# Optimization experiments

Hardware: AMD Instinct MI355X
Metric: run time of the kernel (lower is better)

## Reference

```python
import math
import jax, jax.numpy as jnp
import numpy as np

B, T, D_MODEL, H, D = 2, 1024, 1024, 16, 64
NUM_LEVELS = int(math.ceil(math.log2(T + 1))) + 1  # 12 for max_seq_len=1024


def _fenwick_level(idx):
    return (idx & -idx).bit_length() - 1


def build_fenwick_masks(T, num_levels):
    """NumPy replica of the torch build_fenwick_masks; returns [L, T, T] float32."""
    j_to_nodes = {}
    for j in range(1, T + 1):
        nodes = []
        idx = j
        while idx <= T:
            nodes.append((idx, _fenwick_level(idx)))
            idx += idx & -idx
        j_to_nodes[j] = nodes
    t_to_query_nodes = {}
    for t in range(1, T + 1):
        s = set()
        idx = t
        while idx > 0:
            s.add(idx)
            idx -= idx & -idx
        t_to_query_nodes[t] = s
    masks = np.zeros((num_levels, T, T), dtype=np.float32)
    for t in range(1, T + 1):
        qn = t_to_query_nodes[t]
        for j in range(1, t + 1):
            for node_idx, node_level in j_to_nodes[j]:
                if node_idx in qn:
                    masks[min(node_level, num_levels - 1), t - 1, j - 1] = 1.0
                    break
    return masks


def setup_inputs() -> dict:
    key = jax.random.key(0)
    ks = jax.random.split(key, 8)
    s = 0.02
    return {
        "x": jax.random.normal(ks[0], (B, T, D_MODEL), jnp.float32),
        "qw": jax.random.normal(ks[1], (D_MODEL, H * D), jnp.float32) * s,
        "qb": jnp.zeros((H * D,), jnp.float32),
        "kw": jax.random.normal(ks[2], (D_MODEL, H * D), jnp.float32) * s,
        "kb": jnp.zeros((H * D,), jnp.float32),
        "vw": jax.random.normal(ks[3], (D_MODEL, H * D), jnp.float32) * s,
        "vb": jnp.zeros((H * D,), jnp.float32),
        "lw": jax.random.normal(ks[4], (D_MODEL, H * NUM_LEVELS), jnp.float32) * s,
        "lb": jnp.zeros((H * NUM_LEVELS,), jnp.float32),
        "ow": jax.random.normal(ks[5], (H * D, D_MODEL), jnp.float32) * s,
        "ob": jnp.zeros((D_MODEL,), jnp.float32),
        "level_masks": jnp.asarray(build_fenwick_masks(T, NUM_LEVELS)),
    }


def reference(x, qw, qb, kw, kb, vw, vb, lw, lb, ow, ob, level_masks):
    b, t, _ = x.shape
    phi = lambda a: jax.nn.elu(a) + 1.0  # ELU+1 feature map
    # projections -> [B, H, T, D]
    Q = (x @ qw + qb).reshape(b, t, H, D).transpose(0, 2, 1, 3)
    K = (x @ kw + kb).reshape(b, t, H, D).transpose(0, 2, 1, 3)
    V = (x @ vw + vb).reshape(b, t, H, D).transpose(0, 2, 1, 3)
    Qp, Kp = phi(Q), phi(K)
    # per-level mixing weights: [B, H, T, L]
    logits = (x @ lw + lb).reshape(b, t, H, NUM_LEVELS).transpose(0, 2, 1, 3)
    w = jax.nn.softmax(logits, axis=-1)
    # scores are level-independent in the original; compute once
    S = jnp.einsum('bhid,bhjd->bhij', Qp, Kp)
    # sum_l w_l * mask_l folded into one weighted mask: [B, H, T, T]
    Mw = jnp.einsum('bhil,lij->bhij', w, level_masks)
    Sm = S * Mw
    num = jnp.einsum('bhij,bhjd->bhid', Sm, V)
    den = jnp.maximum(jnp.sum(Sm, axis=-1, keepdims=True), 1e-6)
    out = (num / den).transpose(0, 2, 1, 3).reshape(b, t, H * D)
    return out @ ow + ob
```

## Files before the change

### kernel.cpp

```cpp
#include <hip/hip_runtime.h>
#include <math.h>

typedef __bf16 bf16;
typedef __attribute__((ext_vector_type(4))) __bf16 bf16x4;
typedef __attribute__((ext_vector_type(8))) __bf16 bf16x8;
typedef __attribute__((ext_vector_type(4))) float f32x4;

#define B_SZ 2
#define T_SZ 1024
#define DM_SZ 1024
#define H_SZ 16
#define D_SZ 64
#define L_SZ 12
#define M_ROWS 2048
#define N_PAD 3328

__device__ __forceinline__ f32x4 mfma_16x16x32(bf16x8 a, bf16x8 b, f32x4 c) {
  return __builtin_amdgcn_mfma_f32_16x16x32_bf16(a, b, c, 0, 0, 0);
}

__device__ __forceinline__ void gload_lds16(const bf16* g, bf16* l) {
  __builtin_amdgcn_global_load_lds((const __attribute__((address_space(1))) void*)g,
                                   (__attribute__((address_space(3))) void*)l,
                                   16, 0, 0);
}

__global__ __launch_bounds__(256) void k_prep(
    const float* __restrict__ x, bf16* __restrict__ xb,
    const float* __restrict__ qw, const float* __restrict__ kw,
    const float* __restrict__ vw, const float* __restrict__ ow,
    const float* __restrict__ lw,
    bf16* __restrict__ wqkvT, bf16* __restrict__ owT) {
  const int u = blockIdx.x;
  const int t = threadIdx.x;
  if (u >= 1072) {
    const size_t base = (size_t)(u - 1072) * 8192 + t * 32;
#pragma unroll
    for (int c = 0; c < 4; ++c) {
      const float* p = x + base + c * 8;
      f32x4 a = *(const f32x4*)p;
      f32x4 b = *(const f32x4*)(p + 4);
      bf16x8 o;
#pragma unroll
      for (int e = 0; e < 4; ++e) { o[e] = (bf16)a[e]; o[e + 4] = (bf16)b[e]; }
      *(bf16x8*)(xb + base + c * 8) = o;
    }
    return;
  }
  __shared__ __align__(16) bf16 tile[64][66];
  const float* in; bf16* out; int C = 1024, tx, ty;
  if (u < 1024) {
    const int z = u >> 8, id = u & 255;
    tx = id & 15; ty = id >> 4;
    if (z == 0)      { in = qw; out = wqkvT; }
    else if (z == 1) { in = kw; out = wqkvT + (size_t)1024 * DM_SZ; }
    else if (z == 2) { in = vw; out = wqkvT + (size_t)2048 * DM_SZ; }
    else             { in = ow; out = owT; }
  } else {
    const int id = u - 1024;
    tx = id % 3; ty = id / 3;
    in = lw; out = wqkvT + (size_t)3072 * DM_SZ; C = 192;
  }
  const int tc = tx * 64, tr = ty * 64;
  const int r = t >> 2;
  const int c4 = (t & 3) << 4;
  const float* src = in + (size_t)(tr + r) * C + tc + c4;
  f32x4 f0 = *(const f32x4*)(src);
  f32x4 f1 = *(const f32x4*)(src + 4);
  f32x4 f2 = *(const f32x4*)(src + 8);
  f32x4 f3 = *(const f32x4*)(src + 12);
#pragma unroll
  for (int e = 0; e < 4; ++e) {
    tile[r][c4 + e]      = (bf16)f0[e];
    tile[r][c4 + 4 + e]  = (bf16)f1[e];
    tile[r][c4 + 8 + e]  = (bf16)f2[e];
    tile[r][c4 + 12 + e] = (bf16)f3[e];
  }
  __syncthreads();
  bf16x8 w0, w1;
#pragma unroll
  for (int e = 0; e < 8; ++e) { w0[e] = tile[c4 + e][r]; w1[e] = tile[c4 + 8 + e][r]; }
  bf16* dst = out + (size_t)(tc + r) * DM_SZ + tr + c4;
  *(bf16x8*)(dst) = w0;
  *(bf16x8*)(dst + 8) = w1;
}

__global__ __launch_bounds__(256) void k_gemm_qkvl(
    const bf16* __restrict__ A, const bf16* __restrict__ Wt,
    const float* __restrict__ qb, const float* __restrict__ kb,
    const float* __restrict__ vb, const float* __restrict__ lb,
    bf16* __restrict__ Qp, bf16* __restrict__ Kp,
    bf16* __restrict__ VTg, float* __restrict__ logit) {
  __shared__ __align__(16) char smem[24576];
  bf16* As = (bf16*)smem;
  bf16* Bs = As + 8192;
  const int nb = blockIdx.x * 64;
  const int mb = blockIdx.y * 128;
  const int t = threadIdx.x;
  const int wv = t >> 6;
  const int lane = t & 63;
  const int l16 = lane & 15;
  const int quad = lane >> 4;
  const int wm = wv * 32;
  const int trow = t >> 3;
  const int tcol = (t & 7) * 8;

  const f32x4 zero4 = {0.f, 0.f, 0.f, 0.f};
  f32x4 acc[2][4];
#pragma unroll
  for (int i = 0; i < 2; ++i)
#pragma unroll
    for (int j = 0; j < 4; ++j) acc[i][j] = zero4;

  const bf16* ag = A + (size_t)(mb + trow) * DM_SZ + tcol;
  const bf16* bg = Wt + (size_t)(nb + trow) * DM_SZ + tcol;

  for (int k0 = 0; k0 < DM_SZ; k0 += 64) {
    __syncthreads();
#pragma unroll
    for (int i = 0; i < 4; ++i)
      gload_lds16(ag + (size_t)i * 32 * DM_SZ + k0, As + i * 2048 + t * 8);
#pragma unroll
    for (int i = 0; i < 2; ++i)
      gload_lds16(bg + (size_t)i * 32 * DM_SZ + k0, Bs + i * 2048 + t * 8);
    __syncthreads();
#pragma unroll
    for (int ks = 0; ks < 2; ++ks) {
      bf16x8 af0 = *(const bf16x8*)(As + (wm + l16) * 64 + ks * 32 + quad * 8);
      bf16x8 af1 = *(const bf16x8*)(As + (wm + 16 + l16) * 64 + ks * 32 + quad * 8);
#pragma unroll
      for (int ni = 0; ni < 4; ++ni) {
        bf16x8 bfr = *(const bf16x8*)(Bs + (ni * 16 + l16) * 64 + ks * 32 + quad * 8);
        acc[0][ni] = mfma_16x16x32(af0, bfr, acc[0][ni]);
        acc[1][ni] = mfma_16x16x32(af1, bfr, acc[1][ni]);
      }
    }
  }

  const int seg = nb >> 10;
  if (seg < 2) {
    const float* bias = seg == 0 ? qb : kb;
    bf16* outp = seg == 0 ? Qp : Kp;
    const int c0 = nb & 1023;
#pragma unroll
    for (int ni = 0; ni < 4; ++ni) {
      const int col = c0 + ni * 16 + l16;
      const float bv = bias[col];
#pragma unroll
      for (int mi = 0; mi < 2; ++mi) {
#pragma unroll
        for (int r = 0; r < 4; ++r) {
          const int row = mb + wm + mi * 16 + quad * 4 + r;
          float v = acc[mi][ni][r] + bv;
          v = (v > 0.f) ? (v + 1.f) : __expf(v);
          outp[(size_t)row * DM_SZ + col] = (bf16)v;
        }
      }
    }
  } else if (seg == 2) {
    bf16* Trt = (bf16*)smem;
    const int cb = nb - 2048;
    __syncthreads();
#pragma unroll
    for (int ni = 0; ni < 4; ++ni) {
      const int nloc = ni * 16 + l16;
      const float bv = vb[cb + nloc];
#pragma unroll
      for (int mi = 0; mi < 2; ++mi) {
        const int mloc = wm + mi * 16 + quad * 4;
        bf16x4 pk;
#pragma unroll
        for (int r = 0; r < 4; ++r) pk[r] = (bf16)(acc[mi][ni][r] + bv);
        *(bf16x4*)&Trt[nloc * 136 + mloc] = pk;
      }
    }
    __syncthreads();
    const int dn = t >> 2, ch = t & 3;
    const int bq = mb >> 10;
    const int m0g = mb & 1023;
    bf16* dst = VTg + ((size_t)(bq * 1024 + cb + dn)) * T_SZ + m0g + ch * 32;
    const bf16* srcl = Trt + dn * 136 + ch * 32;
    *(bf16x8*)(dst) = *(const bf16x8*)(srcl);
    *(bf16x8*)(dst + 8) = *(const bf16x8*)(srcl + 8);
    *(bf16x8*)(dst + 16) = *(const bf16x8*)(srcl + 16);
    *(bf16x8*)(dst + 24) = *(const bf16x8*)(srcl + 24);
  } else {
    const int lc0 = nb - 3072;
#pragma unroll
    for (int ni = 0; ni < 4; ++ni) {
      const int lcol = lc0 + ni * 16 + l16;
      if (lcol < H_SZ * L_SZ) {
        const float bv = lb[lcol];
#pragma unroll
        for (int mi = 0; mi < 2; ++mi) {
#pragma unroll
          for (int r = 0; r < 4; ++r) {
            const int row = mb + wm + mi * 16 + quad * 4 + r;
            logit[(size_t)row * (H_SZ * L_SZ) + lcol] = acc[mi][ni][r] + bv;
          }
        }
      }
    }
  }
}

__global__ __launch_bounds__(256) void k_attn(const bf16* __restrict__ Qp,
                                              const bf16* __restrict__ Kp,
                                              const bf16* __restrict__ VTg,
                                              const float* __restrict__ Lg,
                                              bf16* __restrict__ O) {
  __shared__ __align__(16) bf16 Ks[64][80];
  __shared__ __align__(16) bf16 VTs[64][80];
  __shared__ __align__(16) bf16 Pl[4][16][80];
  __shared__ float Ws[64 * L_SZ];

  const int idx = blockIdx.x;
  const int s = idx >> 5;
  const int bh = idx & 31;
  const int it = (s < 8) ? (15 - s) : (s - 8);
  const int b = bh >> 4;
  const int h = bh & 15;
  const int i0 = it * 64;
  const int t = threadIdx.x;
  const int wv = t >> 6;
  const int lane = t & 63;
  const int l16 = lane & 15;
  const int quad = lane >> 4;
  const int m0 = wv * 16;

  const size_t base_bt = (size_t)b * T_SZ;

  const bf16* qptr = Qp + (base_bt + i0 + m0 + l16) * DM_SZ + h * 64 + quad * 8;
  const bf16x8 aq0 = *(const bf16x8*)(qptr);
  const bf16x8 aq1 = *(const bf16x8*)(qptr + 32);

  if (t < 64) {
    const float* lp = Lg + (base_bt + i0 + t) * (H_SZ * L_SZ) + h * L_SZ;
    float v[L_SZ];
    float m = -1e30f;
#pragma unroll
    for (int l = 0; l < L_SZ; ++l) { v[l] = lp[l]; m = fmaxf(m, v[l]); }
    float sum = 0.f;
#pragma unroll
    for (int l = 0; l < L_SZ; ++l) { v[l] = __expf(v[l] - m); sum += v[l]; }
    const float inv = 1.f / sum;
#pragma unroll
    for (int l = 0; l < L_SZ; ++l) Ws[t * L_SZ + l] = v[l] * inv;
  }

  const f32x4 zero4 = {0.f, 0.f, 0.f, 0.f};
  f32x4 accn[4];
#pragma unroll
  for (int tn = 0; tn < 4; ++tn) accn[tn] = zero4;
  float den[4] = {0.f, 0.f, 0.f, 0.f};

  const int sr = t >> 2;
  const int sc = (t & 3) << 4;
  const int il_base = m0 + quad * 4;

  const bf16* vtrow = VTg + ((size_t)bh * 64 + sr) * T_SZ;

  for (int jt = 0; jt <= it; ++jt) {
    const int j0 = jt * 64;
    const bf16* kpg = Kp + (base_bt + j0 + sr) * DM_SZ + h * 64 + sc;
    bf16x8 k0v = *(const bf16x8*)(kpg);
    bf16x8 k1v = *(const bf16x8*)(kpg + 8);
    const bf16* vpg = vtrow + j0 + sc;
    bf16x8 v0v = *(const bf16x8*)(vpg);
    bf16x8 v1v = *(const bf16x8*)(vpg + 8);
    __syncthreads();
    *(bf16x8*)&Ks[sr][sc] = k0v;
    *(bf16x8*)&Ks[sr][sc + 8] = k1v;
    *(bf16x8*)&VTs[sr][sc] = v0v;
    *(bf16x8*)&VTs[sr][sc + 8] = v1v;
    __syncthreads();

    f32x4 sacc[4];
#pragma unroll
    for (int tn = 0; tn < 4; ++tn) {
      sacc[tn] = zero4;
      bf16x8 bk0 = *(const bf16x8*)&Ks[tn * 16 + l16][quad * 8];
      bf16x8 bk1 = *(const bf16x8*)&Ks[tn * 16 + l16][32 + quad * 8];
      sacc[tn] = mfma_16x16x32(aq0, bk0, sacc[tn]);
      sacc[tn] = mfma_16x16x32(aq1, bk1, sacc[tn]);
    }

    if (jt < it) {
      const int lvlA = 6 + (31 - __clz((unsigned)(it ^ jt)));
      const int lvlB = 6 + (31 - __clz((unsigned)((it + 1) ^ jt)));
      float wrow[4];
#pragma unroll
      for (int r = 0; r < 4; ++r) {
        const int il = il_base + r;
        wrow[r] = Ws[il * L_SZ + ((il == 63) ? lvlB : lvlA)];
      }
#pragma unroll
      for (int tn = 0; tn < 4; ++tn) {
#pragma unroll
        for (int r = 0; r < 4; ++r) {
          const float p = sacc[tn][r] * wrow[r];
          den[r] += p;
          Pl[wv][quad * 4 + r][(tn * 16 + l16) ^ (quad << 4)] = (bf16)p;
        }
      }
    } else {
#pragma unroll
      for (int tn = 0; tn < 4; ++tn) {
#pragma unroll
        for (int r = 0; r < 4; ++r) {
          const int il = il_base + r;
          const int ig = i0 + il;
          const int jg = j0 + tn * 16 + l16;
          float p = 0.f;
          if (jg <= ig) {
            const int lvl = 31 - __clz((unsigned)((ig + 1) ^ jg));
            p = sacc[tn][r] * Ws[il * L_SZ + lvl];
          }
          den[r] += p;
          Pl[wv][quad * 4 + r][(tn * 16 + l16) ^ (quad << 4)] = (bf16)p;
        }
      }
    }

#pragma unroll
    for (int ks = 0; ks < 2; ++ks) {
      bf16x8 apf = *(const bf16x8*)&Pl[wv][l16][(ks * 32 + quad * 8) ^ ((l16 >> 2) << 4)];
#pragma unroll
      for (int tn = 0; tn < 4; ++tn) {
        bf16x8 bvf = *(const bf16x8*)&VTs[tn * 16 + l16][ks * 32 + quad * 8];
        accn[tn] = mfma_16x16x32(apf, bvf, accn[tn]);
      }
    }
  }

#pragma unroll
  for (int r = 0; r < 4; ++r) {
    float d = den[r];
    d += __shfl_xor(d, 1, 64);
    d += __shfl_xor(d, 2, 64);
    d += __shfl_xor(d, 4, 64);
    d += __shfl_xor(d, 8, 64);
    den[r] = fmaxf(d, 1e-6f);
  }

#pragma unroll
  for (int tn = 0; tn < 4; ++tn) {
#pragma unroll
    for (int r = 0; r < 4; ++r) {
      const int il = il_base + r;
      O[(base_bt + i0 + il) * DM_SZ + h * 64 + tn * 16 + l16] =
          (bf16)(accn[tn][r] / den[r]);
    }
  }
}

__global__ __launch_bounds__(256) void k_gemm_out(const bf16* __restrict__ A,
                                                  const bf16* __restrict__ Wt,
                                                  const float* __restrict__ ob,
                                                  float* __restrict__ out) {
  __shared__ __align__(16) bf16 As[64 * 64];
  __shared__ __align__(16) bf16 Bs[64 * 64];
  const int nb = (blockIdx.x & 15) * 64;
  const int mb = (blockIdx.x >> 4) * 64;
  const int t = threadIdx.x;
  const int wv = t >> 6;
  const int lane = t & 63;
  const int l16 = lane & 15;
  const int quad = lane >> 4;
  const int wm = wv * 16;
  const int trow = t >> 3;
  const int tcol = (t & 7) * 8;

  const f32x4 zero4 = {0.f, 0.f, 0.f, 0.f};
  f32x4 acc[4];
#pragma unroll
  for (int j = 0; j < 4; ++j) acc[j] = zero4;

  const bf16* ag = A + (size_t)(mb + trow) * DM_SZ + tcol;
  const bf16* bg = Wt + (size_t)(nb + trow) * DM_SZ + tcol;

  for (int k0 = 0; k0 < DM_SZ; k0 += 64) {
    __syncthreads();
    gload_lds16(ag + k0, As + t * 8);
    gload_lds16(ag + (size_t)32 * DM_SZ + k0, As + 2048 + t * 8);
    gload_lds16(bg + k0, Bs + t * 8);
    gload_lds16(bg + (size_t)32 * DM_SZ + k0, Bs + 2048 + t * 8);
    __syncthreads();
#pragma unroll
    for (int ks = 0; ks < 2; ++ks) {
      bf16x8 af = *(const bf16x8*)(As + (wm + l16) * 64 + ks * 32 + quad * 8);
#pragma unroll
      for (int ni = 0; ni < 4; ++ni) {
        bf16x8 bfr = *(const bf16x8*)(Bs + (ni * 16 + l16) * 64 + ks * 32 + quad * 8);
        acc[ni] = mfma_16x16x32(af, bfr, acc[ni]);
      }
    }
  }
#pragma unroll
  for (int ni = 0; ni < 4; ++ni) {
    const int col = nb + ni * 16 + l16;
    const float bv = ob[col];
#pragma unroll
    for (int r = 0; r < 4; ++r) {
      const int row = mb + wm + quad * 4 + r;
      out[(size_t)row * DM_SZ + col] = acc[ni][r] + bv;
    }
  }
}

extern "C" void kernel_launch(void* const* d_in, const int* in_sizes, int n_in,
                              void* d_out, int out_size, void* d_ws, size_t ws_size,
                              hipStream_t stream) {
  (void)in_sizes; (void)n_in; (void)out_size; (void)ws_size;
  const float* x  = (const float*)d_in[0];
  const float* qw = (const float*)d_in[1];
  const float* qb = (const float*)d_in[2];
  const float* kw = (const float*)d_in[3];
  const float* kb = (const float*)d_in[4];
  const float* vw = (const float*)d_in[5];
  const float* vb = (const float*)d_in[6];
  const float* lw = (const float*)d_in[7];
  const float* lb = (const float*)d_in[8];
  const float* ow = (const float*)d_in[9];
  const float* ob = (const float*)d_in[10];

  char* ws = (char*)d_ws;
  size_t off = 0;
  auto alloc = [&](size_t bytes) -> char* {
    char* p = ws + off;
    off += (bytes + 255) & ~(size_t)255;
    return p;
  };
  bf16* xb     = (bf16*)alloc((size_t)M_ROWS * DM_SZ * 2);
  bf16* wqkvT  = (bf16*)alloc((size_t)N_PAD * DM_SZ * 2);
  bf16* owT    = (bf16*)alloc((size_t)DM_SZ * DM_SZ * 2);
  bf16* Qp     = (bf16*)alloc((size_t)M_ROWS * DM_SZ * 2);
  bf16* Kpb    = (bf16*)alloc((size_t)M_ROWS * DM_SZ * 2);
  bf16* VTg    = (bf16*)alloc((size_t)M_ROWS * DM_SZ * 2);
  bf16* attn   = (bf16*)alloc((size_t)M_ROWS * DM_SZ * 2);
  float* logit = (float*)alloc((size_t)M_ROWS * H_SZ * L_SZ * 4);

  const dim3 blk(256);
  k_prep<<<dim3(1328), blk, 0, stream>>>(x, xb, qw, kw, vw, ow, lw, wqkvT, owT);
  k_gemm_qkvl<<<dim3(N_PAD / 64, M_ROWS / 128), blk, 0, stream>>>(
      xb, wqkvT, qb, kb, vb, lb, Qp, Kpb, VTg, logit);
  k_attn<<<dim3((T_SZ / 64) * B_SZ * H_SZ), blk, 0, stream>>>(Qp, Kpb, VTg, logit, attn);
  k_gemm_out<<<dim3(512), blk, 0, stream>>>(attn, owT, ob, (float*)d_out);
}
```

Measured before the change: 184.1 us.

## Replace off-diagonal attention tiles with Fenwick-block linear-attention state matmuls

Uses the fact that off-diagonal tiles share one weight per row within each Fenwick block. For those blocks the kernel now forms a per-block K^T V state (64x64) and a K column sum, then applies Q·state, instead of computing scores tile by tile. The QKV GEMM also writes a transposed K and per-64-row K sums to support this. The state is rebuilt per block of tiles rather than cached, and it is rounded to bf16 before the Q multiply, which may change accuracy.

After: 191.4 us. 1.04x slower.

```diff
diff --git a/kernel.cpp b/kernel.cpp
--- a/kernel.cpp
+++ b/kernel.cpp
@@ -89,8 +89,8 @@
     const bf16* __restrict__ A, const bf16* __restrict__ Wt,
     const float* __restrict__ qb, const float* __restrict__ kb,
     const float* __restrict__ vb, const float* __restrict__ lb,
-    bf16* __restrict__ Qp, bf16* __restrict__ Kp,
-    bf16* __restrict__ VTg, float* __restrict__ logit) {
+    bf16* __restrict__ Qp, bf16* __restrict__ Kp, bf16* __restrict__ KTg,
+    bf16* __restrict__ VTg, float* __restrict__ K1g, float* __restrict__ logit) {
   __shared__ __align__(16) char smem[24576];
   bf16* As = (bf16*)smem;
   bf16* Bs = As + 8192;
@@ -138,14 +138,12 @@
   }
 
   const int seg = nb >> 10;
-  if (seg < 2) {
-    const float* bias = seg == 0 ? qb : kb;
-    bf16* outp = seg == 0 ? Qp : Kp;
+  if (seg == 0) {
     const int c0 = nb & 1023;
 #pragma unroll
     for (int ni = 0; ni < 4; ++ni) {
       const int col = c0 + ni * 16 + l16;
-      const float bv = bias[col];
+      const float bv = qb[col];
 #pragma unroll
       for (int mi = 0; mi < 2; ++mi) {
 #pragma unroll
@@ -153,9 +151,53 @@
           const int row = mb + wm + mi * 16 + quad * 4 + r;
           float v = acc[mi][ni][r] + bv;
           v = (v > 0.f) ? (v + 1.f) : __expf(v);
-          outp[(size_t)row * DM_SZ + col] = (bf16)v;
+          Qp[(size_t)row * DM_SZ + col] = (bf16)v;
         }
       }
+    }
+  } else if (seg == 1) {
+    bf16* Trt = (bf16*)smem;
+    const int c0 = nb - 1024;
+    const int h = c0 >> 6;
+    const int bq = mb >> 10;
+    const int m0g = mb & 1023;
+    const int bh = bq * 16 + h;
+    __syncthreads();
+#pragma unroll
+    for (int ni = 0; ni < 4; ++ni) {
+      const int nloc = ni * 16 + l16;
+      const float bv = kb[c0 + nloc];
+#pragma unroll
+      for (int mi = 0; mi < 2; ++mi) {
+        const int mloc = wm + mi * 16 + quad * 4;
+        bf16x4 pk;
+#pragma unroll
+        for (int r = 0; r < 4; ++r) {
+          float v = acc[mi][ni][r] + bv;
+          v = (v > 0.f) ? (v + 1.f) : __expf(v);
+          pk[r] = (bf16)v;
+          Kp[(size_t)(mb + mloc + r) * DM_SZ + c0 + nloc] = (bf16)v;
+        }
+        *(bf16x4*)&Trt[nloc * 136 + mloc] = pk;
+      }
+    }
+    __syncthreads();
+    {
+      const int dn = t >> 2, ch = t & 3;
+      bf16* dst = KTg + ((size_t)(bh * 64 + dn)) * T_SZ + m0g + ch * 32;
+      const bf16* srcl = Trt + dn * 136 + ch * 32;
+      *(bf16x8*)(dst) = *(const bf16x8*)(srcl);
+      *(bf16x8*)(dst + 8) = *(const bf16x8*)(srcl + 8);
+      *(bf16x8*)(dst + 16) = *(const bf16x8*)(srcl + 16);
+      *(bf16x8*)(dst + 24) = *(const bf16x8*)(srcl + 24);
+    }
+    if (t < 128) {
+      const int d = t >> 1, half = t & 1;
+      const bf16* rowp = Trt + d * 136 + half * 64;
+      float s = 0.f;
+#pragma unroll
+      for (int e = 0; e < 64; ++e) s += (float)rowp[e];
+      K1g[((size_t)bh * 16 + (m0g >> 6) + half) * 64 + d] = s;
     }
   } else if (seg == 2) {
     bf16* Trt = (bf16*)smem;
@@ -206,19 +248,21 @@
 
 __global__ __launch_bounds__(256) void k_attn(const bf16* __restrict__ Qp,
                                               const bf16* __restrict__ Kp,
+                                              const bf16* __restrict__ KTg,
                                               const bf16* __restrict__ VTg,
+                                              const float* __restrict__ K1g,
                                               const float* __restrict__ Lg,
                                               bf16* __restrict__ O) {
-  __shared__ __align__(16) bf16 Ks[64][80];
-  __shared__ __align__(16) bf16 VTs[64][80];
+  __shared__ float Ws[64 * L_SZ];
+  __shared__ __align__(16) bf16 Mlds[64 * 72];
+  __shared__ float K1Lds[64];
   __shared__ __align__(16) bf16 Pl[4][16][80];
-  __shared__ float Ws[64 * L_SZ];
 
   const int idx = blockIdx.x;
   const int s = idx >> 5;
   const int bh = idx & 31;
   const int it = (s < 8) ? (15 - s) : (s - 8);
-  const int b = bh >> 4;
+  const int b_ = bh >> 4;
   const int h = bh & 15;
   const int i0 = it * 64;
   const int t = threadIdx.x;
@@ -228,7 +272,7 @@
   const int quad = lane >> 4;
   const int m0 = wv * 16;
 
-  const size_t base_bt = (size_t)b * T_SZ;
+  const size_t base_bt = (size_t)b_ * T_SZ;
 
   const bf16* qptr = Qp + (base_bt + i0 + m0 + l16) * DM_SZ + h * 64 + quad * 8;
   const bf16x8 aq0 = *(const bf16x8*)(qptr);
@@ -247,87 +291,130 @@
 #pragma unroll
     for (int l = 0; l < L_SZ; ++l) Ws[t * L_SZ + l] = v[l] * inv;
   }
+  __syncthreads();
 
   const f32x4 zero4 = {0.f, 0.f, 0.f, 0.f};
   f32x4 accn[4];
 #pragma unroll
   for (int tn = 0; tn < 4; ++tn) accn[tn] = zero4;
-  float den[4] = {0.f, 0.f, 0.f, 0.f};
-
-  const int sr = t >> 2;
-  const int sc = (t & 3) << 4;
+  float den_a = 0.f;
+  float dden[4] = {0.f, 0.f, 0.f, 0.f};
+
   const int il_base = m0 + quad * 4;
-
-  const bf16* vtrow = VTg + ((size_t)bh * 64 + sr) * T_SZ;
-
-  for (int jt = 0; jt <= it; ++jt) {
-    const int j0 = jt * 64;
-    const bf16* kpg = Kp + (base_bt + j0 + sr) * DM_SZ + h * 64 + sc;
-    bf16x8 k0v = *(const bf16x8*)(kpg);
-    bf16x8 k1v = *(const bf16x8*)(kpg + 8);
-    const bf16* vpg = vtrow + j0 + sc;
-    bf16x8 v0v = *(const bf16x8*)(vpg);
-    bf16x8 v1v = *(const bf16x8*)(vpg + 8);
-    __syncthreads();
-    *(bf16x8*)&Ks[sr][sc] = k0v;
-    *(bf16x8*)&Ks[sr][sc + 8] = k1v;
-    *(bf16x8*)&VTs[sr][sc] = v0v;
-    *(bf16x8*)&VTs[sr][sc + 8] = v1v;
-    __syncthreads();
-
+  const bf16* c1a = VTg + ((size_t)(bh * 64 + m0 + l16)) * T_SZ;
+  const bf16* c1b = KTg + ((size_t)(bh * 64)) * T_SZ;
+
+#pragma unroll
+  for (int b = 3; b >= 0; --b) {
+    if (!(it & (1 << b))) continue;
+    const int pfx = (it >> (b + 1)) << (b + 1);
+    const int hi = pfx + (1 << b);
+    f32x4 macc[4];
+#pragma unroll
+    for (int ni = 0; ni < 4; ++ni) macc[ni] = zero4;
+    for (int kt = pfx; kt < hi; ++kt) {
+      const int k0 = kt * 64;
+      bf16x8 a0 = *(const bf16x8*)(c1a + k0 + quad * 8);
+      bf16x8 a1 = *(const bf16x8*)(c1a + k0 + 32 + quad * 8);
+#pragma unroll
+      for (int ni = 0; ni < 4; ++ni) {
+        const bf16* brow = c1b + (size_t)(ni * 16 + l16) * T_SZ + k0;
+        bf16x8 b0 = *(const bf16x8*)(brow + quad * 8);
+        bf16x8 b1 = *(const bf16x8*)(brow + 32 + quad * 8);
+        macc[ni] = mfma_16x16x32(a0, b0, macc[ni]);
+        macc[ni] = mfma_16x16x32(a1, b1, macc[ni]);
+      }
+    }
+    __syncthreads();
+#pragma unroll
+    for (int ni = 0; ni < 4; ++ni) {
+#pragma unroll
+      for (int r = 0; r < 4; ++r)
+        Mlds[(m0 + quad * 4 + r) * 72 + ni * 16 + l16] = (bf16)macc[ni][r];
+    }
+    if (t < 64) {
+      float ssum = 0.f;
+      for (int kt = pfx; kt < hi; ++kt)
+        ssum += K1g[((size_t)bh * 16 + kt) * 64 + t];
+      K1Lds[t] = ssum;
+    }
+    __syncthreads();
+    f32x4 tmp[4];
+#pragma unroll
+    for (int ni = 0; ni < 4; ++ni) tmp[ni] = zero4;
+#pragma unroll
+    for (int ks = 0; ks < 2; ++ks) {
+      const bf16x8 aqk = ks ? aq1 : aq0;
+#pragma unroll
+      for (int ni = 0; ni < 4; ++ni) {
+        bf16x8 bm = *(const bf16x8*)(Mlds + (ni * 16 + l16) * 72 + ks * 32 + quad * 8);
+        tmp[ni] = mfma_16x16x32(aqk, bm, tmp[ni]);
+      }
+    }
+    const int lvlA = 6 + b;
+    const int lvlB = 6 + (31 - __clz((unsigned)((it + 1) ^ pfx)));
+    float wrow[4];
+#pragma unroll
+    for (int r = 0; r < 4; ++r) {
+      const int il = il_base + r;
+      wrow[r] = Ws[il * L_SZ + ((il == 63) ? lvlB : lvlA)];
+    }
+#pragma unroll
+    for (int ni = 0; ni < 4; ++ni)
+#pragma unroll
+      for (int r = 0; r < 4; ++r) accn[ni][r] += wrow[r] * tmp[ni][r];
+    {
+      const int ilA = m0 + l16;
+      const float wA = Ws[ilA * L_SZ + ((ilA == 63) ? lvlB : lvlA)];
+      float dot = 0.f;
+#pragma unroll
+      for (int e = 0; e < 8; ++e)
+        dot += (float)aq0[e] * K1Lds[quad * 8 + e] +
+               (float)aq1[e] * K1Lds[32 + quad * 8 + e];
+      dot += __shfl_xor(dot, 16, 64);
+      dot += __shfl_xor(dot, 32, 64);
+      den_a += wA * dot;
+    }
+  }
+
+  {
+    const int j0 = i0;
     f32x4 sacc[4];
 #pragma unroll
+    for (int tn = 0; tn < 4; ++tn) sacc[tn] = zero4;
+#pragma unroll
+    for (int ks = 0; ks < 2; ++ks) {
+      const bf16x8 aqk = ks ? aq1 : aq0;
+#pragma unroll
+      for (int tn = 0; tn < 4; ++tn) {
+        bf16x8 bk = *(const bf16x8*)(Kp + (base_bt + j0 + tn * 16 + l16) * DM_SZ +
+                                     h * 64 + ks * 32 + quad * 8);
+        sacc[tn] = mfma_16x16x32(aqk, bk, sacc[tn]);
+      }
+    }
+#pragma unroll
     for (int tn = 0; tn < 4; ++tn) {
-      sacc[tn] = zero4;
-      bf16x8 bk0 = *(const bf16x8*)&Ks[tn * 16 + l16][quad * 8];
-      bf16x8 bk1 = *(const bf16x8*)&Ks[tn * 16 + l16][32 + quad * 8];
-      sacc[tn] = mfma_16x16x32(aq0, bk0, sacc[tn]);
-      sacc[tn] = mfma_16x16x32(aq1, bk1, sacc[tn]);
-    }
-
-    if (jt < it) {
-      const int lvlA = 6 + (31 - __clz((unsigned)(it ^ jt)));
-      const int lvlB = 6 + (31 - __clz((unsigned)((it + 1) ^ jt)));
-      float wrow[4];
 #pragma unroll
       for (int r = 0; r < 4; ++r) {
         const int il = il_base + r;
-        wrow[r] = Ws[il * L_SZ + ((il == 63) ? lvlB : lvlA)];
-      }
-#pragma unroll
-      for (int tn = 0; tn < 4; ++tn) {
-#pragma unroll
-        for (int r = 0; r < 4; ++r) {
-          const float p = sacc[tn][r] * wrow[r];
-          den[r] += p;
-          Pl[wv][quad * 4 + r][(tn * 16 + l16) ^ (quad << 4)] = (bf16)p;
+        const int ig = i0 + il;
+        const int jg = j0 + tn * 16 + l16;
+        float p = 0.f;
+        if (jg <= ig) {
+          const int lvl = 31 - __clz((unsigned)((ig + 1) ^ jg));
+          p = sacc[tn][r] * Ws[il * L_SZ + lvl];
         }
-      }
-    } else {
-#pragma unroll
-      for (int tn = 0; tn < 4; ++tn) {
-#pragma unroll
-        for (int r = 0; r < 4; ++r) {
-          const int il = il_base + r;
-          const int ig = i0 + il;
-          const int jg = j0 + tn * 16 + l16;
-          float p = 0.f;
-          if (jg <= ig) {
-            const int lvl = 31 - __clz((unsigned)((ig + 1) ^ jg));
-            p = sacc[tn][r] * Ws[il * L_SZ + lvl];
-          }
-          den[r] += p;
-          Pl[wv][quad * 4 + r][(tn * 16 + l16) ^ (quad << 4)] = (bf16)p;
-        }
-      }
-    }
-
+        dden[r] += p;
+        Pl[wv][quad * 4 + r][(tn * 16 + l16) ^ (quad << 4)] = (bf16)p;
+      }
+    }
 #pragma unroll
     for (int ks = 0; ks < 2; ++ks) {
       bf16x8 apf = *(const bf16x8*)&Pl[wv][l16][(ks * 32 + quad * 8) ^ ((l16 >> 2) << 4)];
 #pragma unroll
       for (int tn = 0; tn < 4; ++tn) {
-        bf16x8 bvf = *(const bf16x8*)&VTs[tn * 16 + l16][ks * 32 + quad * 8];
+        bf16x8 bvf = *(const bf16x8*)(VTg + ((size_t)(bh * 64 + tn * 16 + l16)) * T_SZ +
+                                      j0 + ks * 32 + quad * 8);
         accn[tn] = mfma_16x16x32(apf, bvf, accn[tn]);
       }
     }
@@ -335,12 +422,13 @@
 
 #pragma unroll
   for (int r = 0; r < 4; ++r) {
-    float d = den[r];
+    float d = dden[r];
     d += __shfl_xor(d, 1, 64);
     d += __shfl_xor(d, 2, 64);
     d += __shfl_xor(d, 4, 64);
     d += __shfl_xor(d, 8, 64);
-    den[r] = fmaxf(d, 1e-6f);
+    const float dg = __shfl(den_a, quad * 4 + r, 64);
+    dden[r] = fmaxf(d + dg, 1e-6f);
   }
 
 #pragma unroll
@@ -349,7 +437,7 @@
     for (int r = 0; r < 4; ++r) {
       const int il = il_base + r;
       O[(base_bt + i0 + il) * DM_SZ + h * 64 + tn * 16 + l16] =
-          (bf16)(accn[tn][r] / den[r]);
+          (bf16)(accn[tn][r] / dden[r]);
     }
   }
 }
@@ -436,14 +524,17 @@
   bf16* owT    = (bf16*)alloc((size_t)DM_SZ * DM_SZ * 2);
   bf16* Qp     = (bf16*)alloc((size_t)M_ROWS * DM_SZ * 2);
   bf16* Kpb    = (bf16*)alloc((size_t)M_ROWS * DM_SZ * 2);
+  bf16* KTg    = (bf16*)alloc((size_t)M_ROWS * DM_SZ * 2);
   bf16* VTg    = (bf16*)alloc((size_t)M_ROWS * DM_SZ * 2);
   bf16* attn   = (bf16*)alloc((size_t)M_ROWS * DM_SZ * 2);
+  float* K1g   = (float*)alloc((size_t)32 * 16 * 64 * 4);
   float* logit = (float*)alloc((size_t)M_ROWS * H_SZ * L_SZ * 4);
 
   const dim3 blk(256);
   k_prep<<<dim3(1328), blk, 0, stream>>>(x, xb, qw, kw, vw, ow, lw, wqkvT, owT);
   k_gemm_qkvl<<<dim3(N_PAD / 64, M_ROWS / 128), blk, 0, stream>>>(
-      xb, wqkvT, qb, kb, vb, lb, Qp, Kpb, VTg, logit);
-  k_attn<<<dim3((T_SZ / 64) * B_SZ * H_SZ), blk, 0, stream>>>(Qp, Kpb, VTg, logit, attn);
+      xb, wqkvT, qb, kb, vb, lb, Qp, Kpb, KTg, VTg, K1g, logit);
+  k_attn<<<dim3((T_SZ / 64) * B_SZ * H_SZ), blk, 0, stream>>>(
+      Qp, Kpb, KTg, VTg, K1g, logit, attn);
   k_gemm_out<<<dim3(512), blk, 0, stream>>>(attn, owT, ob, (float*)d_out);
 }
```
